# Performance work log

Measured on AMD Instinct MI355X. Metric: run time of the kernel, lower is better.

Reference implementation:

```python
import jax, jax.numpy as jnp
import numpy as np

N_ATOMS = 8192
N_PAIR = 131072
F = 128
N_HEAD = 8
FH = F // N_HEAD            # 16
DEGREES = [1, 2, 3]
N_DEG = len(DEGREES)
REPEATS = np.array([2 * l + 1 for l in DEGREES])  # [3,5,7]
M_TOT = int(REPEATS.sum())  # 15
K_RBF = 32
H_FILT = 64
FILT_OUT = 2 * N_DEG * F    # 768


def setup_inputs() -> dict:
    key = jax.random.key(0)
    ks = jax.random.split(key, 12)
    x = jax.random.normal(ks[0], (N_ATOMS, F), dtype=jnp.float32)
    rbf_ij = jax.random.uniform(ks[1], (N_PAIR, K_RBF), dtype=jnp.float32)
    sph_ij = jax.random.normal(ks[2], (N_PAIR, M_TOT), dtype=jnp.float32)
    phi_r_cut = jax.random.uniform(ks[3], (N_PAIR,), dtype=jnp.float32)
    idx_i = jnp.sort(jax.random.randint(ks[4], (N_PAIR,), 0, N_ATOMS))
    idx_j = jax.random.randint(ks[5], (N_PAIR,), 0, N_ATOMS)
    pair_mask = jnp.ones((N_PAIR,), dtype=jnp.float32)
    # params (lecun-normal-ish scaling)
    W_Q = jax.random.normal(ks[6], (N_DEG, N_HEAD, FH, FH), dtype=jnp.float32) / np.sqrt(FH)
    W_K = jax.random.normal(ks[7], (N_DEG, N_HEAD, FH, FH), dtype=jnp.float32) / np.sqrt(FH)
    a = jax.random.normal(ks[8], (N_DEG, N_HEAD, 2 * FH), dtype=jnp.float32) / np.sqrt(2 * FH)
    mlp_w1 = jax.random.normal(ks[9], (K_RBF, H_FILT), dtype=jnp.float32) / np.sqrt(K_RBF)
    mlp_b1 = jnp.zeros((H_FILT,), dtype=jnp.float32)
    mlp_w2 = jax.random.normal(ks[10], (H_FILT, FILT_OUT), dtype=jnp.float32) / np.sqrt(H_FILT)
    mlp_b2 = jnp.zeros((FILT_OUT,), dtype=jnp.float32)
    return {"x": x, "rbf_ij": rbf_ij, "sph_ij": sph_ij, "phi_r_cut": phi_r_cut,
            "idx_i": idx_i, "idx_j": idx_j, "pair_mask": pair_mask,
            "W_Q": W_Q, "W_K": W_K, "a": a,
            "mlp_w1": mlp_w1, "mlp_b1": mlp_b1, "mlp_w2": mlp_w2, "mlp_b2": mlp_b2}


def reference(x, rbf_ij, sph_ij, phi_r_cut, idx_i, idx_j, pair_mask,
              W_Q, W_K, a, mlp_w1, mlp_b1, mlp_w2, mlp_b2):
    n = x.shape[0]
    x_head = x.reshape(n, N_HEAD, FH)                       # (n, h, fh)
    # per-atom, per-degree, per-head linear maps
    Q = jnp.einsum('dhij,nhj->ndhi', W_Q, x_head)           # (n, d, h, fh)
    K = jnp.einsum('dhij,nhj->ndhi', W_K, x_head)
    m4 = pair_mask[:, None, None, None]
    Q_i = Q[idx_i] * m4                                     # (p, d, h, fh)
    K_j = K[idx_j] * m4
    QK = jnp.concatenate((Q_i, K_j), axis=-1)               # (p, d, h, 2fh)
    # radial filter MLP
    h1 = jax.nn.silu(rbf_ij @ mlp_w1 + mlp_b1)
    W_ij = (h1 @ mlp_w2 + mlp_b2).reshape(-1, N_DEG, N_HEAD, 2 * FH)
    W_ij = W_ij * phi_r_cut[:, None, None, None]
    # attention logits (non-softmax)
    alpha = jnp.sum(QK * W_ij * a[None], axis=-1)           # (p, d, h)
    alpha = jnp.repeat(alpha, REPEATS, axis=1, total_repeat_length=M_TOT)  # (p, m, h)
    alpha = alpha / jnp.sqrt(jnp.float32(FH))               # att_scale
    # outer product with spherical harmonics + scatter
    x_j = x_head[idx_j] * pair_mask[:, None, None]          # (p, h, fh)
    z = alpha[..., None] * (sph_ij[:, :, None, None] * x_j[:, None, :, :])  # (p, m, h, fh)
    z = z.reshape(z.shape[0], M_TOT, F)                     # (p, m, F)
    return jax.ops.segment_sum(z, idx_i, num_segments=n)    # (n, m, F)
```

## Files before the change

### kernel.cpp

```cpp
#include <hip/hip_runtime.h>
#include <hip/hip_bf16.h>

#define N_ATOMS 8192
#define N_PAIR  131072
#define F       128
#define N_HEAD  8
#define FH      16
#define N_DEG   3
#define M_TOT   15
#define K_RBF   32
#define H_FILT  64
#define FILT_OUT 768
#define NDH     24
#define ATB     4

typedef __attribute__((ext_vector_type(8))) unsigned short u16x8;

__device__ __forceinline__ float bf2f(unsigned short u) {
    return __uint_as_float(((unsigned)u) << 16);
}
__device__ __forceinline__ unsigned short f2bfbits(float f) {
    __hip_bfloat16 b = __float2bfloat16(f);
    return *reinterpret_cast<unsigned short*>(&b);
}

__global__ __launch_bounds__(256) void k_front(
    const int* __restrict__ idx_i, int* __restrict__ row_start,
    int* __restrict__ counts, int* __restrict__ cnt2,
    const float* __restrict__ WQ, const float* __restrict__ WK,
    const float* __restrict__ avec, const float* __restrict__ W2,
    const float* __restrict__ b2, float* __restrict__ Wc, float* __restrict__ bc,
    const float* __restrict__ rbf, const float* __restrict__ W1,
    const float* __restrict__ b1, unsigned short* __restrict__ h1)
{
    __shared__ __align__(16) char smem[16896];
    int tid = threadIdx.x;
    int bx = blockIdx.x;
    if (bx < 32) {
        int t = bx * 256 + tid;
        counts[t] = 0; cnt2[t] = 0;
        return;
    }
    bx -= 32;
    if (bx < 48) {
        float* w2s = (float*)smem;
        float* wsm = (float*)(smem + 4096);
        float* as  = (float*)(smem + 5120);
        float* b2s = (float*)(smem + 5184);
        int side = bx / NDH, dh = bx % NDH;
        int d = dh >> 3, h = dh & 7;
        int colbase = d * 256 + h * 32 + side * 16;
        const float* W = (side == 0) ? WQ : WK;
        for (int e = tid; e < 1024; e += 256)
            w2s[e] = W2[(e >> 4) * FILT_OUT + colbase + (e & 15)];
        wsm[tid] = W[((d * 8 + h) * 16) * 16 + tid];
        if (tid < 16) { as[tid] = avec[dh * 32 + side * 16 + tid]; b2s[tid] = b2[colbase + tid]; }
        __syncthreads();
        for (int o = tid; o < 1024; o += 256) {
            int k = o >> 4, j = o & 15;
            float s = 0.f;
            #pragma unroll
            for (int c = 0; c < 16; ++c) s += w2s[k * 16 + c] * as[c] * wsm[c * 16 + j];
            Wc[((size_t)bx * 64 + k) * 16 + j] = s;
        }
        if (tid < 16) {
            float s = 0.f;
            #pragma unroll
            for (int c = 0; c < 16; ++c) s += b2s[c] * as[c] * wsm[c * 16 + tid];
            bc[bx * 16 + tid] = s;
        }
        return;
    }
    bx -= 48;
    if (bx < 512) {
        int p = bx * 256 + tid;
        int ii = idx_i[p];
        int prev = (p == 0) ? -1 : idx_i[p - 1];
        for (int a = prev + 1; a <= ii; ++a) row_start[a] = p;
        if (p == N_PAIR - 1) {
            for (int a = ii + 1; a <= N_ATOMS; ++a) row_start[a] = N_PAIR;
        }
        return;
    }
    bx -= 512;
    {
        float* w1s  = (float*)smem;
        float* b1s  = (float*)(smem + 8192);
        float* rbfs = (float*)(smem + 8448);
        int p0 = bx * 64;
        for (int e = tid; e < K_RBF * H_FILT; e += 256) w1s[e] = W1[e];
        if (tid < H_FILT) b1s[tid] = b1[tid];
        for (int e = tid; e < 64 * K_RBF; e += 256)
            rbfs[(e >> 5) * 33 + (e & 31)] = rbf[(size_t)p0 * K_RBF + e];
        __syncthreads();
        int pp = tid >> 2;
        int kbase = (tid & 3) * 16;
        float acc[16];
        #pragma unroll
        for (int q = 0; q < 16; ++q) acc[q] = b1s[kbase + q];
        for (int c = 0; c < K_RBF; ++c) {
            float r = rbfs[pp * 33 + c];
            #pragma unroll
            for (int q = 0; q < 16; ++q) acc[q] += r * w1s[c * 64 + kbase + q];
        }
        u16x8 o0, o1;
        #pragma unroll
        for (int q = 0; q < 8; ++q) {
            float s0 = acc[q];     o0[q] = f2bfbits(s0 / (1.f + __expf(-s0)));
            float s1 = acc[q + 8]; o1[q] = f2bfbits(s1 / (1.f + __expf(-s1)));
        }
        unsigned short* hp = h1 + (size_t)(p0 + pp) * 64 + kbase;
        *reinterpret_cast<u16x8*>(hp) = o0;
        *reinterpret_cast<u16x8*>(hp + 8) = o1;
    }
}

__global__ void k_hist(const int* __restrict__ idx_j, int* __restrict__ counts) {
    int p = blockIdx.x * 256 + threadIdx.x;
    if (p < N_PAIR) atomicAdd(&counts[idx_j[p]], 1);
}

__global__ __launch_bounds__(1024) void k_scan(const int* __restrict__ counts,
                                               int* __restrict__ offsets) {
    __shared__ int ts[1024];
    int tid = threadIdx.x;
    int base = tid * 8;
    int v[8]; int tot = 0;
    #pragma unroll
    for (int q = 0; q < 8; ++q) { v[q] = counts[base + q]; tot += v[q]; }
    ts[tid] = tot; __syncthreads();
    for (int off = 1; off < 1024; off <<= 1) {
        int t2 = (tid >= off) ? ts[tid - off] : 0;
        __syncthreads();
        ts[tid] += t2;
        __syncthreads();
    }
    int excl = ts[tid] - tot;
    #pragma unroll
    for (int q = 0; q < 8; ++q) { offsets[base + q] = excl; excl += v[q]; }
    if (tid == 1023) offsets[N_ATOMS] = ts[1023];
}

__global__ void k_place(const int* __restrict__ idx_j, const int* __restrict__ offsets,
                        int* __restrict__ cnt2, int* __restrict__ sorted,
                        int* __restrict__ rank) {
    int p = blockIdx.x * 256 + threadIdx.x;
    if (p < N_PAIR) {
        int j = idx_j[p];
        int pos = offsets[j] + atomicAdd(&cnt2[j], 1);
        sorted[pos] = p;
        rank[p] = pos;
    }
}

__global__ __launch_bounds__(256) void k_gfused(
    const float* __restrict__ x, const float* __restrict__ Wc,
    const float* __restrict__ bc,
    __hip_bfloat16* __restrict__ Gq, __hip_bfloat16* __restrict__ Gk,
    float* __restrict__ bq, float* __restrict__ bk)
{
    int bx = blockIdx.x;
    int by = blockIdx.y;
    int side = by / NDH, dh = by % NDH;
    int h = dh & 7;
    int n0 = bx * 64;
    __shared__ float xh[64][17];
    __shared__ float bcs[16];
    int tid = threadIdx.x;
    for (int e = tid; e < 64 * 16; e += 256)
        xh[e >> 4][e & 15] = x[(size_t)(n0 + (e >> 4)) * F + h * 16 + (e & 15)];
    if (tid < 16) bcs[tid] = bc[by * 16 + tid];
    int k = tid & 63, wv = tid >> 6;
    float wcr[16];
    const float* wp = Wc + ((size_t)by * 64 + k) * 16;
    #pragma unroll
    for (int j = 0; j < 16; ++j) wcr[j] = wp[j];
    __syncthreads();
    __hip_bfloat16* G = (side == 0) ? Gq : Gk;
    #pragma unroll 4
    for (int it = 0; it < 16; ++it) {
        int at = wv * 16 + it;
        float acc = 0.f;
        #pragma unroll
        for (int j = 0; j < 16; ++j) acc += wcr[j] * xh[at][j];
        G[(size_t)(n0 + at) * 1536 + dh * 64 + k] = __float2bfloat16(acc);
    }
    if (tid < 64) {
        float* B = (side == 0) ? bq : bk;
        float s = 0.f;
        #pragma unroll
        for (int j = 0; j < 16; ++j) s += bcs[j] * xh[tid][j];
        B[(n0 + tid) * NDH + dh] = s;
    }
}

__device__ __forceinline__ void stage_h1f(float (*h1f)[72],
                                          const unsigned short* __restrict__ h1,
                                          const int* ps, int tid) {
    for (int e = tid; e < 64 * 32; e += 256) {
        int slot = e >> 5, kp = e & 31;
        unsigned d = *reinterpret_cast<const unsigned*>(h1 + (size_t)ps[slot] * 64 + kp * 2);
        float2 f;
        f.x = __uint_as_float(d << 16);
        f.y = __uint_as_float(d & 0xFFFF0000u);
        *reinterpret_cast<float2*>(&h1f[slot][kp * 2]) = f;
    }
}

__device__ __forceinline__ float dot8u(uint4 g, float4 h0, float4 h1v) {
    float p;
    p  = __uint_as_float(g.x << 16) * h0.x + __uint_as_float(g.x & 0xFFFF0000u) * h0.y;
    p += __uint_as_float(g.y << 16) * h0.z + __uint_as_float(g.y & 0xFFFF0000u) * h0.w;
    p += __uint_as_float(g.z << 16) * h1v.x + __uint_as_float(g.z & 0xFFFF0000u) * h1v.y;
    p += __uint_as_float(g.w << 16) * h1v.z + __uint_as_float(g.w & 0xFFFF0000u) * h1v.w;
    return p;
}

__global__ __launch_bounds__(256) void k_alphak2(
    const int* __restrict__ sorted, const int* __restrict__ idx_j,
    const unsigned short* __restrict__ h1,
    const __hip_bfloat16* __restrict__ Gk, const float* __restrict__ bk,
    unsigned short* __restrict__ alphaKs)
{
    __shared__ __align__(16) float h1f[64][72];
    __shared__ float als[64][24];
    __shared__ int ps[64];
    __shared__ int js[64];
    int tid = threadIdx.x;
    int c0 = blockIdx.x * 64;
    if (tid < 64) {
        int pid = sorted[c0 + tid];
        ps[tid] = pid;
        js[tid] = idx_j[pid];
    }
    __syncthreads();
    stage_h1f(h1f, h1, ps, tid);
    __syncthreads();
    const unsigned short* GkU = reinterpret_cast<const unsigned short*>(Gk);
    int seg = tid & 7;
    for (int t = 0; t < 12; ++t) {
        int base = t * 1024 + tid;
        int ds0 = base >> 3, ds1 = (base + 256) >> 3,
            ds2 = (base + 512) >> 3, ds3 = (base + 768) >> 3;
        int s0 = ds0 / 24, d0 = ds0 - s0 * 24;
        int s1 = ds1 / 24, d1 = ds1 - s1 * 24;
        int s2 = ds2 / 24, d2 = ds2 - s2 * 24;
        int s3 = ds3 / 24, d3 = ds3 - s3 * 24;
        uint4 g0 = *reinterpret_cast<const uint4*>(GkU + (size_t)js[s0] * 1536 + d0 * 64 + seg * 8);
        uint4 g1 = *reinterpret_cast<const uint4*>(GkU + (size_t)js[s1] * 1536 + d1 * 64 + seg * 8);
        uint4 g2 = *reinterpret_cast<const uint4*>(GkU + (size_t)js[s2] * 1536 + d2 * 64 + seg * 8);
        uint4 g3 = *reinterpret_cast<const uint4*>(GkU + (size_t)js[s3] * 1536 + d3 * 64 + seg * 8);
        float p0 = dot8u(g0, *reinterpret_cast<const float4*>(&h1f[s0][seg * 8]),
                             *reinterpret_cast<const float4*>(&h1f[s0][seg * 8 + 4]));
        float p1 = dot8u(g1, *reinterpret_cast<const float4*>(&h1f[s1][seg * 8]),
                             *reinterpret_cast<const float4*>(&h1f[s1][seg * 8 + 4]));
        float p2 = dot8u(g2, *reinterpret_cast<const float4*>(&h1f[s2][seg * 8]),
                             *reinterpret_cast<const float4*>(&h1f[s2][seg * 8 + 4]));
        float p3 = dot8u(g3, *reinterpret_cast<const float4*>(&h1f[s3][seg * 8]),
                             *reinterpret_cast<const float4*>(&h1f[s3][seg * 8 + 4]));
        p0 += __shfl_xor(p0, 1); p1 += __shfl_xor(p1, 1);
        p2 += __shfl_xor(p2, 1); p3 += __shfl_xor(p3, 1);
        p0 += __shfl_xor(p0, 2); p1 += __shfl_xor(p1, 2);
        p2 += __shfl_xor(p2, 2); p3 += __shfl_xor(p3, 2);
        p0 += __shfl_xor(p0, 4); p1 += __shfl_xor(p1, 4);
        p2 += __shfl_xor(p2, 4); p3 += __shfl_xor(p3, 4);
        if (seg == 0) {
            als[s0][d0] = p0; als[s1][d1] = p1;
            als[s2][d2] = p2; als[s3][d3] = p3;
        }
    }
    __syncthreads();
    for (int e = tid; e < 64 * 24; e += 256) {
        int slot = e / 24, dh = e - slot * 24;
        float val = als[slot][dh] + bk[js[slot] * NDH + dh];
        alphaKs[(size_t)c0 * 24 + e] = f2bfbits(val);
    }
}

__global__ __launch_bounds__(256) void k_alphaA2(
    const int* __restrict__ idx_i, const int* __restrict__ rank,
    const float* __restrict__ phi, const float* __restrict__ mask,
    const unsigned short* __restrict__ h1,
    const __hip_bfloat16* __restrict__ Gq, const float* __restrict__ bq,
    const unsigned short* __restrict__ alphaKs,
    float* __restrict__ alphaF)
{
    __shared__ __align__(16) float h1f[64][72];
    __shared__ float als[64][24];
    __shared__ int is[64];
    __shared__ int rks[64];
    __shared__ float pms[64];
    __shared__ int psn[64];
    int tid = threadIdx.x;
    int p0 = blockIdx.x * 64;
    if (tid < 64) {
        int p = p0 + tid;
        is[tid] = idx_i[p];
        rks[tid] = rank[p];
        float mk = mask[p];
        pms[tid] = phi[p] * mk * mk * 0.25f;
        psn[tid] = p;
    }
    __syncthreads();
    stage_h1f(h1f, h1, psn, tid);
    __syncthreads();
    const unsigned short* GqU = reinterpret_cast<const unsigned short*>(Gq);
    int seg = tid & 7;
    for (int t = 0; t < 12; ++t) {
        int base = t * 1024 + tid;
        int ds0 = base >> 3, ds1 = (base + 256) >> 3,
            ds2 = (base + 512) >> 3, ds3 = (base + 768) >> 3;
        int s0 = ds0 / 24, d0 = ds0 - s0 * 24;
        int s1 = ds1 / 24, d1 = ds1 - s1 * 24;
        int s2 = ds2 / 24, d2 = ds2 - s2 * 24;
        int s3 = ds3 / 24, d3 = ds3 - s3 * 24;
        uint4 g0 = *reinterpret_cast<const uint4*>(GqU + (size_t)is[s0] * 1536 + d0 * 64 + seg * 8);
        uint4 g1 = *reinterpret_cast<const uint4*>(GqU + (size_t)is[s1] * 1536 + d1 * 64 + seg * 8);
        uint4 g2 = *reinterpret_cast<const uint4*>(GqU + (size_t)is[s2] * 1536 + d2 * 64 + seg * 8);
        uint4 g3 = *reinterpret_cast<const uint4*>(GqU + (size_t)is[s3] * 1536 + d3 * 64 + seg * 8);
        float p0v = dot8u(g0, *reinterpret_cast<const float4*>(&h1f[s0][seg * 8]),
                              *reinterpret_cast<const float4*>(&h1f[s0][seg * 8 + 4]));
        float p1v = dot8u(g1, *reinterpret_cast<const float4*>(&h1f[s1][seg * 8]),
                              *reinterpret_cast<const float4*>(&h1f[s1][seg * 8 + 4]));
        float p2v = dot8u(g2, *reinterpret_cast<const float4*>(&h1f[s2][seg * 8]),
                              *reinterpret_cast<const float4*>(&h1f[s2][seg * 8 + 4]));
        float p3v = dot8u(g3, *reinterpret_cast<const float4*>(&h1f[s3][seg * 8]),
                              *reinterpret_cast<const float4*>(&h1f[s3][seg * 8 + 4]));
        p0v += __shfl_xor(p0v, 1); p1v += __shfl_xor(p1v, 1);
        p2v += __shfl_xor(p2v, 1); p3v += __shfl_xor(p3v, 1);
        p0v += __shfl_xor(p0v, 2); p1v += __shfl_xor(p1v, 2);
        p2v += __shfl_xor(p2v, 2); p3v += __shfl_xor(p3v, 2);
        p0v += __shfl_xor(p0v, 4); p1v += __shfl_xor(p1v, 4);
        p2v += __shfl_xor(p2v, 4); p3v += __shfl_xor(p3v, 4);
        if (seg == 0) {
            als[s0][d0] = p0v; als[s1][d1] = p1v;
            als[s2][d2] = p2v; als[s3][d3] = p3v;
        }
    }
    __syncthreads();
    for (int e = tid; e < 64 * 24; e += 256) {
        int slot = e / 24, dh = e - slot * 24;
        float val = als[slot][dh] + bq[is[slot] * NDH + dh]
                  + bf2f(alphaKs[(size_t)rks[slot] * 24 + dh]);
        alphaF[(size_t)p0 * 24 + e] = val * pms[slot];
    }
}

__global__ __launch_bounds__(256) void k_aggr6(
    const float* __restrict__ x, const float* __restrict__ sph,
    const int* __restrict__ idx_i, const int* __restrict__ idx_j,
    const float* __restrict__ alphaF,
    const int* __restrict__ row_start, float* __restrict__ out)
{
    int a0 = blockIdx.x * ATB;
    int tid = threadIdx.x;
    int f = tid & 127, grp = tid >> 7, h = f >> 4;

    __shared__ float als[32][24];
    __shared__ float sls[32][16];
    __shared__ int   iis[32];
    __shared__ int   jjs[32];
    __shared__ int   rs[ATB + 1];

    if (tid <= ATB) rs[tid] = row_start[a0 + tid];
    __syncthreads();
    int pstart = rs[0], pend = rs[ATB];

    float acc[8];
    #pragma unroll
    for (int m = 0; m < 8; ++m) acc[m] = 0.f;
    int cur = -1;

#define FLUSH(CUR)                                                        \
    { size_t ob = (size_t)(CUR) * (M_TOT * F) + f;                        \
      if (grp == 0) {                                                     \
          _Pragma("unroll")                                               \
          for (int m = 0; m < 8; ++m) out[ob + m * 128] = acc[m];         \
      } else {                                                            \
          _Pragma("unroll")                                               \
          for (int m = 0; m < 7; ++m) out[ob + (8 + m) * 128] = acc[m];   \
      } }

#define AGG_STEP(Q, XV)                                                   \
    { int ia = iis[Q];                                                    \
      if (ia != cur) {                                                    \
          if (cur >= 0) FLUSH(cur);                                       \
          cur = ia;                                                       \
          _Pragma("unroll")                                               \
          for (int m = 0; m < 8; ++m) acc[m] = 0.f;                       \
      }                                                                   \
      if (grp == 0) {                                                     \
          float t0 = als[Q][h] * (XV);                                    \
          float t1 = als[Q][8 + h] * (XV);                                \
          acc[0] += t0 * sls[Q][0];                                       \
          acc[1] += t0 * sls[Q][1];                                       \
          acc[2] += t0 * sls[Q][2];                                       \
          _Pragma("unroll")                                               \
          for (int m = 3; m < 8; ++m) acc[m] += t1 * sls[Q][m];           \
      } else {                                                            \
          float t2 = als[Q][16 + h] * (XV);                               \
          _Pragma("unroll")                                               \
          for (int m = 0; m < 7; ++m) acc[m] += t2 * sls[Q][8 + m];       \
      } }

    for (int pc = pstart; pc < pend; pc += 32) {
        int nb = min(32, pend - pc);
        __syncthreads();
        if (tid < nb) {
            int p = pc + tid;
            iis[tid] = idx_i[p];
            jjs[tid] = idx_j[p];
        }
        for (int e = tid; e < nb * 24; e += 256)
            als[e / 24][e % 24] = alphaF[(size_t)pc * 24 + e];
        for (int e = tid; e < nb * 15; e += 256)
            sls[e / 15][e % 15] = sph[(size_t)pc * 15 + e];
        __syncthreads();
        float xa = 0.f, xb = 0.f, xc = 0.f, xd = 0.f;
        if (nb > 0) xa = x[(size_t)jjs[0] * F + f];
        if (nb > 1) xb = x[(size_t)jjs[1] * F + f];
        if (nb > 2) xc = x[(size_t)jjs[2] * F + f];
        if (nb > 3) xd = x[(size_t)jjs[3] * F + f];
        for (int qg = 0; qg < nb; qg += 4) {
            float ya = 0.f, yb = 0.f, yc = 0.f, yd = 0.f;
            int nq = qg + 4;
            if (nq < nb) {
                ya = x[(size_t)jjs[nq] * F + f];
                if (nq + 1 < nb) yb = x[(size_t)jjs[nq + 1] * F + f];
                if (nq + 2 < nb) yc = x[(size_t)jjs[nq + 2] * F + f];
                if (nq + 3 < nb) yd = x[(size_t)jjs[nq + 3] * F + f];
            }
            AGG_STEP(qg, xa);
            if (qg + 1 < nb) AGG_STEP(qg + 1, xb);
            if (qg + 2 < nb) AGG_STEP(qg + 2, xc);
            if (qg + 3 < nb) AGG_STEP(qg + 3, xd);
            xa = ya; xb = yb; xc = yc; xd = yd;
        }
    }
    if (cur >= 0) FLUSH(cur);
    for (int a = 0; a < ATB; ++a) {
        if (rs[a] == rs[a + 1]) {
            size_t ob = (size_t)(a0 + a) * (M_TOT * F) + f;
            if (grp == 0) {
                #pragma unroll
                for (int m = 0; m < 8; ++m) out[ob + m * 128] = 0.f;
            } else {
                #pragma unroll
                for (int m = 0; m < 7; ++m) out[ob + (8 + m) * 128] = 0.f;
            }
        }
    }
#undef AGG_STEP
#undef FLUSH
}

extern "C" void kernel_launch(void* const* d_in, const int* in_sizes, int n_in,
                              void* d_out, int out_size, void* d_ws, size_t ws_size,
                              hipStream_t stream) {
    const float* x     = (const float*)d_in[0];
    const float* rbf   = (const float*)d_in[1];
    const float* sph   = (const float*)d_in[2];
    const float* phi   = (const float*)d_in[3];
    const int*   idx_i = (const int*)d_in[4];
    const int*   idx_j = (const int*)d_in[5];
    const float* mask  = (const float*)d_in[6];
    const float* WQ    = (const float*)d_in[7];
    const float* WK    = (const float*)d_in[8];
    const float* av    = (const float*)d_in[9];
    const float* W1    = (const float*)d_in[10];
    const float* b1    = (const float*)d_in[11];
    const float* W2    = (const float*)d_in[12];
    const float* b2    = (const float*)d_in[13];
    float* out = (float*)d_out;
    char* ws = (char*)d_ws;

    __hip_bfloat16* Gq = (__hip_bfloat16*)(ws + 0);
    __hip_bfloat16* Gk = (__hip_bfloat16*)(ws + 25165824);
    float* alphaF = (float*)(ws + 25165824);
    float* bq = (float*)(ws + 50331648);
    float* bk = (float*)(ws + 51118080);
    int* row_start = (int*)(ws + 51904512);
    int* counts    = (int*)(ws + 51937792);
    int* offsets   = (int*)(ws + 51970560);
    int* cnt2      = (int*)(ws + 52003840);
    int* sorted    = (int*)(ws + 52036608);
    int* rank      = (int*)(ws + 52560896);
    unsigned short* h1      = (unsigned short*)(ws + 53085184);
    unsigned short* alphaKs = (unsigned short*)(ws + 69862400);
    float* Wc = (float*)(ws + 76153856);
    float* bc = (float*)(ws + 76350464);

    k_front<<<2640, 256, 0, stream>>>(idx_i, row_start, counts, cnt2,
                                      WQ, WK, av, W2, b2, Wc, bc,
                                      rbf, W1, b1, h1);
    k_hist<<<(N_PAIR + 255) / 256, 256, 0, stream>>>(idx_j, counts);
    k_scan<<<1, 1024, 0, stream>>>(counts, offsets);
    k_place<<<(N_PAIR + 255) / 256, 256, 0, stream>>>(idx_j, offsets, cnt2, sorted, rank);
    k_gfused<<<dim3(N_ATOMS / 64, 48), 256, 0, stream>>>(x, Wc, bc, Gq, Gk, bq, bk);
    k_alphak2<<<N_PAIR / 64, 256, 0, stream>>>(sorted, idx_j, h1, Gk, bk, alphaKs);
    k_alphaA2<<<N_PAIR / 64, 256, 0, stream>>>(idx_i, rank, phi, mask, h1, Gq, bq,
                                               alphaKs, alphaF);
    k_aggr6<<<N_ATOMS / ATB, 256, 0, stream>>>(x, sph, idx_i, idx_j, alphaF,
                                               row_start, out);
}
```

Before: 180.3 us.

## Fold histogram into front kernel and restructure aggregation by atom segments

```diff
diff --git a/kernel.cpp b/kernel.cpp
--- a/kernel.cpp
+++ b/kernel.cpp
@@ -25,8 +25,8 @@
 }
 
 __global__ __launch_bounds__(256) void k_front(
-    const int* __restrict__ idx_i, int* __restrict__ row_start,
-    int* __restrict__ counts, int* __restrict__ cnt2,
+    const int* __restrict__ idx_i, const int* __restrict__ idx_j,
+    int* __restrict__ row_start, int* __restrict__ counts,
     const float* __restrict__ WQ, const float* __restrict__ WK,
     const float* __restrict__ avec, const float* __restrict__ W2,
     const float* __restrict__ b2, float* __restrict__ Wc, float* __restrict__ bc,
@@ -36,12 +36,6 @@
     __shared__ __align__(16) char smem[16896];
     int tid = threadIdx.x;
     int bx = blockIdx.x;
-    if (bx < 32) {
-        int t = bx * 256 + tid;
-        counts[t] = 0; cnt2[t] = 0;
-        return;
-    }
-    bx -= 32;
     if (bx < 48) {
         float* w2s = (float*)smem;
         float* wsm = (float*)(smem + 4096);
@@ -83,6 +77,12 @@
         return;
     }
     bx -= 512;
+    if (bx < 512) {
+        int p = bx * 256 + tid;
+        atomicAdd(&counts[idx_j[p]], 1);
+        return;
+    }
+    bx -= 512;
     {
         float* w1s  = (float*)smem;
         float* b1s  = (float*)(smem + 8192);
@@ -113,11 +113,6 @@
         *reinterpret_cast<u16x8*>(hp) = o0;
         *reinterpret_cast<u16x8*>(hp + 8) = o1;
     }
-}
-
-__global__ void k_hist(const int* __restrict__ idx_j, int* __restrict__ counts) {
-    int p = blockIdx.x * 256 + threadIdx.x;
-    if (p < N_PAIR) atomicAdd(&counts[idx_j[p]], 1);
 }
 
 __global__ __launch_bounds__(1024) void k_scan(const int* __restrict__ counts,
@@ -346,9 +341,9 @@
     }
 }
 
-__global__ __launch_bounds__(256) void k_aggr6(
+__global__ __launch_bounds__(256) void k_aggr7(
     const float* __restrict__ x, const float* __restrict__ sph,
-    const int* __restrict__ idx_i, const int* __restrict__ idx_j,
+    const int* __restrict__ idx_j,
     const float* __restrict__ alphaF,
     const int* __restrict__ row_start, float* __restrict__ out)
 {
@@ -357,8 +352,7 @@
     int f = tid & 127, grp = tid >> 7, h = f >> 4;
 
     __shared__ float als[32][24];
-    __shared__ float sls[32][16];
-    __shared__ int   iis[32];
+    __shared__ __align__(16) float sls[32][16];
     __shared__ int   jjs[32];
     __shared__ int   rs[ATB + 1];
 
@@ -369,7 +363,6 @@
     float acc[8];
     #pragma unroll
     for (int m = 0; m < 8; ++m) acc[m] = 0.f;
-    int cur = -1;
 
 #define FLUSH(CUR)                                                        \
     { size_t ob = (size_t)(CUR) * (M_TOT * F) + f;                        \
@@ -381,63 +374,60 @@
           for (int m = 0; m < 7; ++m) out[ob + (8 + m) * 128] = acc[m];   \
       } }
 
-#define AGG_STEP(Q, XV)                                                   \
-    { int ia = iis[Q];                                                    \
-      if (ia != cur) {                                                    \
-          if (cur >= 0) FLUSH(cur);                                       \
-          cur = ia;                                                       \
-          _Pragma("unroll")                                               \
-          for (int m = 0; m < 8; ++m) acc[m] = 0.f;                       \
-      }                                                                   \
-      if (grp == 0) {                                                     \
-          float t0 = als[Q][h] * (XV);                                    \
-          float t1 = als[Q][8 + h] * (XV);                                \
-          acc[0] += t0 * sls[Q][0];                                       \
-          acc[1] += t0 * sls[Q][1];                                       \
-          acc[2] += t0 * sls[Q][2];                                       \
-          _Pragma("unroll")                                               \
-          for (int m = 3; m < 8; ++m) acc[m] += t1 * sls[Q][m];           \
-      } else {                                                            \
-          float t2 = als[Q][16 + h] * (XV);                               \
-          _Pragma("unroll")                                               \
-          for (int m = 0; m < 7; ++m) acc[m] += t2 * sls[Q][8 + m];       \
-      } }
-
     for (int pc = pstart; pc < pend; pc += 32) {
         int nb = min(32, pend - pc);
         __syncthreads();
-        if (tid < nb) {
-            int p = pc + tid;
-            iis[tid] = idx_i[p];
-            jjs[tid] = idx_j[p];
-        }
+        if (tid < nb) jjs[tid] = idx_j[pc + tid];
         for (int e = tid; e < nb * 24; e += 256)
             als[e / 24][e % 24] = alphaF[(size_t)pc * 24 + e];
         for (int e = tid; e < nb * 15; e += 256)
             sls[e / 15][e % 15] = sph[(size_t)pc * 15 + e];
         __syncthreads();
-        float xa = 0.f, xb = 0.f, xc = 0.f, xd = 0.f;
-        if (nb > 0) xa = x[(size_t)jjs[0] * F + f];
-        if (nb > 1) xb = x[(size_t)jjs[1] * F + f];
-        if (nb > 2) xc = x[(size_t)jjs[2] * F + f];
-        if (nb > 3) xd = x[(size_t)jjs[3] * F + f];
-        for (int qg = 0; qg < nb; qg += 4) {
-            float ya = 0.f, yb = 0.f, yc = 0.f, yd = 0.f;
-            int nq = qg + 4;
-            if (nq < nb) {
-                ya = x[(size_t)jjs[nq] * F + f];
-                if (nq + 1 < nb) yb = x[(size_t)jjs[nq + 1] * F + f];
-                if (nq + 2 < nb) yc = x[(size_t)jjs[nq + 2] * F + f];
-                if (nq + 3 < nb) yd = x[(size_t)jjs[nq + 3] * F + f];
+        #pragma unroll
+        for (int a = 0; a < ATB; ++a) {
+            int s = max(rs[a], pc), en = min(rs[a + 1], pc + nb);
+            if (s < en) {
+                int qs = s - pc, qe = en - pc;
+                if (grp == 0) {
+                    for (int q = qs; q < qe; ++q) {
+                        float xv = x[(size_t)jjs[q] * F + f];
+                        float4 s03 = *reinterpret_cast<const float4*>(&sls[q][0]);
+                        float4 s47 = *reinterpret_cast<const float4*>(&sls[q][4]);
+                        float t0 = als[q][h] * xv;
+                        float t1 = als[q][8 + h] * xv;
+                        acc[0] += t0 * s03.x;
+                        acc[1] += t0 * s03.y;
+                        acc[2] += t0 * s03.z;
+                        acc[3] += t1 * s03.w;
+                        acc[4] += t1 * s47.x;
+                        acc[5] += t1 * s47.y;
+                        acc[6] += t1 * s47.z;
+                        acc[7] += t1 * s47.w;
+                    }
+                } else {
+                    for (int q = qs; q < qe; ++q) {
+                        float xv = x[(size_t)jjs[q] * F + f];
+                        float4 s811  = *reinterpret_cast<const float4*>(&sls[q][8]);
+                        float4 s1215 = *reinterpret_cast<const float4*>(&sls[q][12]);
+                        float t2 = als[q][16 + h] * xv;
+                        acc[0] += t2 * s811.x;
+                        acc[1] += t2 * s811.y;
+                        acc[2] += t2 * s811.z;
+                        acc[3] += t2 * s811.w;
+                        acc[4] += t2 * s1215.x;
+                        acc[5] += t2 * s1215.y;
+                        acc[6] += t2 * s1215.z;
+                    }
+                }
             }
-            AGG_STEP(qg, xa);
-            if (qg + 1 < nb) AGG_STEP(qg + 1, xb);
-            if (qg + 2 < nb) AGG_STEP(qg + 2, xc);
-            if (qg + 3 < nb) AGG_STEP(qg + 3, xd);
-            xa = ya; xb = yb; xc = yc; xd = yd;
-        }
-    }
-    if (cur >= 0) FLUSH(cur);
+            if (rs[a] < rs[a + 1] && rs[a + 1] <= pc + nb && rs[a + 1] > pc) {
+                FLUSH(a0 + a);
+                #pragma unroll
+                for (int m = 0; m < 8; ++m) acc[m] = 0.f;
+            }
+        }
+    }
+    #pragma unroll
     for (int a = 0; a < ATB; ++a) {
         if (rs[a] == rs[a + 1]) {
             size_t ob = (size_t)(a0 + a) * (M_TOT * F) + f;
@@ -450,7 +440,6 @@
             }
         }
     }
-#undef AGG_STEP
 #undef FLUSH
 }
 
@@ -481,8 +470,8 @@
     float* bk = (float*)(ws + 51118080);
     int* row_start = (int*)(ws + 51904512);
     int* counts    = (int*)(ws + 51937792);
-    int* offsets   = (int*)(ws + 51970560);
-    int* cnt2      = (int*)(ws + 52003840);
+    int* cnt2      = (int*)(ws + 51970560);
+    int* offsets   = (int*)(ws + 52003328);
     int* sorted    = (int*)(ws + 52036608);
     int* rank      = (int*)(ws + 52560896);
     unsigned short* h1      = (unsigned short*)(ws + 53085184);
@@ -490,16 +479,15 @@
     float* Wc = (float*)(ws + 76153856);
     float* bc = (float*)(ws + 76350464);
 
-    k_front<<<2640, 256, 0, stream>>>(idx_i, row_start, counts, cnt2,
+    hipMemsetAsync(ws + 51937792, 0, 65536, stream);
+    k_front<<<3120, 256, 0, stream>>>(idx_i, idx_j, row_start, counts,
                                       WQ, WK, av, W2, b2, Wc, bc,
                                       rbf, W1, b1, h1);
-    k_hist<<<(N_PAIR + 255) / 256, 256, 0, stream>>>(idx_j, counts);
     k_scan<<<1, 1024, 0, stream>>>(counts, offsets);
     k_place<<<(N_PAIR + 255) / 256, 256, 0, stream>>>(idx_j, offsets, cnt2, sorted, rank);
     k_gfused<<<dim3(N_ATOMS / 64, 48), 256, 0, stream>>>(x, Wc, bc, Gq, Gk, bq, bk);
     k_alphak2<<<N_PAIR / 64, 256, 0, stream>>>(sorted, idx_j, h1, Gk, bk, alphaKs);
     k_alphaA2<<<N_PAIR / 64, 256, 0, stream>>>(idx_i, rank, phi, mask, h1, Gq, bq,
                                                alphaKs, alphaF);
-    k_aggr6<<<N_ATOMS / ATB, 256, 0, stream>>>(x, sph, idx_i, idx_j, alphaF,
-                                               row_start, out);
-}
+    k_aggr7<<<N_ATOMS / ATB, 256, 0, stream>>>(x, sph, idx_j, alphaF, row_start, out);
+}
```

New measurement: 207.4 us. 15.1% more time.
